# Kernel optimization log

Hardware: AMD Instinct MI355X
Metric: run time of the kernel (lower is better)

The kernel has to match this reference:

```python
import jax, jax.numpy as jnp
import numpy as np

B, T, D_MODEL = 2, 2048, 2048
D_HEAD = 128
H_PER_G = 4
N_GROUPS = D_MODEL // (H_PER_G * D_HEAD)  # 4
ROT_BASE = 10000
EPS = 1e-6


def setup_inputs() -> dict:
    key = jax.random.key(0)
    ks = jax.random.split(key, 5)
    s = D_MODEL ** -0.5
    return {
        "x": jax.random.normal(ks[0], (B, T, D_MODEL), jnp.float32),
        "wq": jax.random.normal(ks[1], (D_MODEL, D_MODEL), jnp.float32) * s,
        "wk": jax.random.normal(ks[2], (D_MODEL, D_MODEL // H_PER_G), jnp.float32) * s,
        "wv": jax.random.normal(ks[3], (D_MODEL, D_MODEL // H_PER_G), jnp.float32) * s,
        "wo": jax.random.normal(ks[4], (D_MODEL, D_MODEL), jnp.float32) * s,
        "gq": jnp.ones((N_GROUPS, H_PER_G, D_HEAD), jnp.float32),
        "gk": jnp.ones((N_GROUPS, D_HEAD), jnp.float32),
    }


def _rmsnorm(t):
    rms = jnp.sqrt(jnp.mean(jnp.square(t), axis=-1, keepdims=True) + EPS)
    return t / rms


def _rope(t):
    # t: [..., length, width]
    length, width = t.shape[-2], t.shape[-1]
    pos = jnp.arange(length)[:, None]                       # [t,1]
    dims = jnp.arange(width // 2)[None, :]                  # [1,d/2]
    ang = jnp.power(float(ROT_BASE), -dims / (width // 2))
    rad = (pos * ang).astype(t.dtype)                       # [t,d/2]
    cos, sin = jnp.cos(rad), jnp.sin(rad)
    even, odd = jnp.split(t, 2, axis=-1)
    return jnp.concatenate([even * cos - odd * sin, even * sin + odd * cos], axis=-1)


def reference(x, wq, wk, wv, wo, gq, gk):
    b, t, _ = x.shape
    q = jnp.einsum('bti,io->bto', x, wq)
    k = jnp.einsum('bti,io->bto', x, wk)
    v = jnp.einsum('bti,io->bto', x, wv)
    # b t (g h d) -> b g h t d ; b t (g d) -> b g t d
    q = q.reshape(b, t, N_GROUPS, H_PER_G, D_HEAD).transpose(0, 2, 3, 1, 4)
    k = k.reshape(b, t, N_GROUPS, D_HEAD).transpose(0, 2, 1, 3)
    v = v.reshape(b, t, N_GROUPS, D_HEAD).transpose(0, 2, 1, 3)
    # QK RMSNorm with gains
    q = _rmsnorm(q) * gq[None, :, :, None, :]
    k = _rmsnorm(k) * gk[None, :, None, :]
    # RoPE
    q = _rope(q)
    k = _rope(k)
    mult = jnp.asarray(D_HEAD ** -0.25, x.dtype)
    s = jnp.einsum('bghid,bgjd->bghij', q * mult, k * mult)
    # causal mask: subtract 1e30 where i < j
    i = jnp.arange(t)[:, None]
    j = jnp.arange(t)[None, :]
    s = s - jnp.asarray(1e30, s.dtype) * (i < j)
    p = jax.nn.softmax(s, axis=-1)
    o = jnp.einsum('bghij,bgjd->bghid', p, v)
    o = o.transpose(0, 3, 1, 2, 4).reshape(b, t, D_MODEL)
    return jnp.einsum('bti,io->bto', o, wo)
```

## Files before the change

### kernel.cpp

```cpp
#include <hip/hip_runtime.h>
#include <cstdint>

typedef unsigned short u16;
typedef __attribute__((ext_vector_type(8))) __bf16 bf16x8;
typedef __attribute__((ext_vector_type(4))) float f32x4;
typedef __attribute__((ext_vector_type(8))) unsigned short u16x8;

#define DEV __device__ __forceinline__

DEV u16 f2bf(float f) {
  __bf16 b = (__bf16)f;
  return __builtin_bit_cast(u16, b);
}
DEV float bf2f(u16 h) { return __uint_as_float(((unsigned)h) << 16); }
DEV float exp2_fast(float x) { float r; asm("v_exp_f32 %0, %1" : "=v"(r) : "v"(x)); return r; }

typedef __attribute__((address_space(1))) void gvoid_t;
typedef __attribute__((address_space(3))) void lvoid_t;

DEV void gload_lds16(const void* g, void* l) {
  __builtin_amdgcn_global_load_lds((gvoid_t*)(void*)(uintptr_t)g,
                                   (lvoid_t*)l, 16, 0, 0);
}

#define B_   2
#define T_   2048
#define DM   2048
#define MROWS (B_*T_)

__global__ void k_convert(const float* __restrict__ in, u16* __restrict__ out, int n4) {
  int i = blockIdx.x * blockDim.x + threadIdx.x;
  if (i >= n4) return;
  float4 v = ((const float4*)in)[i];
  ((ushort4*)out)[i] = make_ushort4(f2bf(v.x), f2bf(v.y), f2bf(v.z), f2bf(v.w));
}

__global__ void k_transpose(const float* __restrict__ in, u16* __restrict__ out, int R, int C) {
  __shared__ float tile[32][33];
  int c0 = blockIdx.x * 32, r0 = blockIdx.y * 32;
  int tx = threadIdx.x, ty = threadIdx.y;
  #pragma unroll
  for (int j = 0; j < 32; j += 8)
    tile[ty + j][tx] = in[(size_t)(r0 + ty + j) * C + c0 + tx];
  __syncthreads();
  #pragma unroll
  for (int j = 0; j < 32; j += 8)
    out[(size_t)(c0 + ty + j) * R + r0 + tx] = f2bf(tile[tx][ty + j]);
}

__global__ void k_rope_table(float2* __restrict__ tab) {
  int i = blockIdx.x * blockDim.x + threadIdx.x;
  int pos = i >> 6, d = i & 63;
  float ang = powf(10000.0f, -(float)d / 64.0f);
  float s, c;
  sincosf((float)pos * ang, &s, &c);
  tab[i] = make_float2(c, s);
}

template <typename OutT>
__global__ __launch_bounds__(256) void k_gemm(
    const u16* __restrict__ A, const u16* __restrict__ BT, OutT* __restrict__ C,
    int M, int N, int K) {
  __shared__ u16 As[128 * 64];
  __shared__ u16 Bs[128 * 64];
  const int tid = threadIdx.x;
  const int w = tid >> 6, lane = tid & 63;
  const int lr = lane & 15, lg = lane >> 4;
  const int m0 = blockIdx.y * 128, n0 = blockIdx.x * 128;
  const int wr = w >> 1, wc = w & 1;
  f32x4 acc[4][4] = {};
  for (int k0 = 0; k0 < K; k0 += 64) {
    __syncthreads();
    #pragma unroll
    for (int i = 0; i < 4; i++) {
      int idx = i * 256 + tid;
      int row = idx >> 3, blk = idx & 7;
      int scol = ((blk ^ (row & 7)) << 3);
      gload_lds16(&A[(size_t)(m0 + row) * K + k0 + scol], &As[(idx & ~63) * 8]);
      gload_lds16(&BT[(size_t)(n0 + row) * K + k0 + scol], &Bs[(idx & ~63) * 8]);
    }
    __syncthreads();
    #pragma unroll
    for (int kk = 0; kk < 2; kk++) {
      bf16x8 af[4], bfr[4];
      #pragma unroll
      for (int m = 0; m < 4; m++) {
        int row = wr * 64 + m * 16 + lr;
        af[m] = *(const bf16x8*)&As[row * 64 + (((kk * 4 + lg) ^ (lr & 7)) << 3)];
      }
      #pragma unroll
      for (int n = 0; n < 4; n++) {
        int row = wc * 64 + n * 16 + lr;
        bfr[n] = *(const bf16x8*)&Bs[row * 64 + (((kk * 4 + lg) ^ (lr & 7)) << 3)];
      }
      #pragma unroll
      for (int m = 0; m < 4; m++)
        #pragma unroll
        for (int n = 0; n < 4; n++)
          acc[m][n] = __builtin_amdgcn_mfma_f32_16x16x32_bf16(af[m], bfr[n], acc[m][n], 0, 0, 0);
    }
  }
  #pragma unroll
  for (int m = 0; m < 4; m++)
    #pragma unroll
    for (int n = 0; n < 4; n++)
      #pragma unroll
      for (int r = 0; r < 4; r++) {
        int row = m0 + wr * 64 + m * 16 + lg * 4 + r;
        int col = n0 + wc * 64 + n * 16 + lr;
        if constexpr (sizeof(OutT) == 2) C[(size_t)row * N + col] = f2bf(acc[m][n][r]);
        else                             C[(size_t)row * N + col] = acc[m][n][r];
      }
}

__global__ void k_norm_rope_q(const u16* __restrict__ qkvf, const float* __restrict__ gq,
                              const float2* __restrict__ tab, u16* __restrict__ qb) {
  int w = threadIdx.x >> 6, lane = threadIdx.x & 63;
  int W = blockIdx.x * 4 + w;
  int h = W & 3, g = (W >> 2) & 3;
  int bt = W >> 4;
  int t = bt & 2047, b = bt >> 11;
  const u16* row = qkvf + (size_t)bt * 3072 + (size_t)(g * 4 + h) * 128;
  float v0 = bf2f(row[lane]);
  float v1 = bf2f(row[lane + 64]);
  float ss = v0 * v0 + v1 * v1;
  #pragma unroll
  for (int off = 1; off < 64; off <<= 1) ss += __shfl_xor(ss, off, 64);
  float inv = 1.0f / sqrtf(ss * (1.0f / 128.0f) + 1e-6f);
  v0 *= inv * gq[(g * 4 + h) * 128 + lane];
  v1 *= inv * gq[(g * 4 + h) * 128 + 64 + lane];
  float2 cs = tab[t * 64 + lane];
  const float sc = 0.1275174f;
  float o0 = (v0 * cs.x - v1 * cs.y) * sc;
  float o1 = (v0 * cs.y + v1 * cs.x) * sc;
  u16* orow = qb + ((size_t)(((b * 4 + g) * 4 + h) * 2048 + t)) * 128;
  orow[lane] = f2bf(o0);
  orow[lane + 64] = f2bf(o1);
}

__global__ void k_norm_rope_k(const u16* __restrict__ qkvf, const float* __restrict__ gk,
                              const float2* __restrict__ tab, u16* __restrict__ kb) {
  int w = threadIdx.x >> 6, lane = threadIdx.x & 63;
  int W = blockIdx.x * 4 + w;
  int g = W & 3;
  int bt = W >> 2;
  int t = bt & 2047, b = bt >> 11;
  const u16* row = qkvf + (size_t)bt * 3072 + 2048 + (size_t)g * 128;
  float v0 = bf2f(row[lane]);
  float v1 = bf2f(row[lane + 64]);
  float ss = v0 * v0 + v1 * v1;
  #pragma unroll
  for (int off = 1; off < 64; off <<= 1) ss += __shfl_xor(ss, off, 64);
  float inv = 1.0f / sqrtf(ss * (1.0f / 128.0f) + 1e-6f);
  v0 *= inv * gk[g * 128 + lane];
  v1 *= inv * gk[g * 128 + 64 + lane];
  float2 cs = tab[t * 64 + lane];
  float o0 = v0 * cs.x - v1 * cs.y;
  float o1 = v0 * cs.y + v1 * cs.x;
  u16* orow = kb + ((size_t)((b * 4 + g) * 2048 + t)) * 128;
  orow[lane] = f2bf(o0);
  orow[lane + 64] = f2bf(o1);
}

__global__ void k_pack_vt(const u16* __restrict__ qkvf, u16* __restrict__ vt) {
  int w = threadIdx.x >> 6, lane = threadIdx.x & 63;
  int W = blockIdx.x * 4 + w;
  int t8 = W & 255, dh = (W >> 8) & 1, bg = W >> 9;
  int b = bg >> 2, g = bg & 3;
  int t0 = t8 * 8;
  int d = dh * 64 + lane;
  u16x8 pack;
  #pragma unroll
  for (int j = 0; j < 8; j++)
    pack[j] = qkvf[(size_t)(b * 2048 + t0 + j) * 3072 + 2560 + g * 128 + d];
  *(u16x8*)&vt[((size_t)(bg * 128 + d)) * 2048 + t0] = pack;
}

DEV void stage_tiles(const u16* kh, const u16* vh, int j0, u16* Kbuf, u16* Vbuf, int tid) {
  #pragma unroll
  for (int i = 0; i < 4; i++) {
    int idx = i * 256 + tid;
    int row = idx >> 4, blk = idx & 15;
    gload_lds16(&kh[(size_t)(j0 + row) * 128 + ((blk ^ (row & 7)) << 3)],
                &Kbuf[(idx & ~63) * 8]);
  }
  #pragma unroll
  for (int i = 0; i < 4; i++) {
    int idx = i * 256 + tid;
    int row = idx >> 3, blk = idx & 7;
    gload_lds16(&vh[(size_t)row * T_ + j0 + ((blk ^ (row & 7)) << 3)],
                &Vbuf[(idx & ~63) * 8]);
  }
}

DEV void attn_tile(const u16* __restrict__ Kc, const u16* __restrict__ Vc,
                   u16* __restrict__ Psw, const bf16x8* qf, f32x4* oacc,
                   float& mrun, float& lsum,
                   int lr, int lg, int w, bool diag) {
  f32x4 s[4] = {};
  #pragma unroll
  for (int kk = 0; kk < 4; kk++) {
    #pragma unroll
    for (int c = 0; c < 4; c++) {
      const int kvr = c * 16 + lr;
      bf16x8 kf = *(const bf16x8*)&Kc[kvr * 128 + (((kk * 4 + lg) ^ (kvr & 7)) << 3)];
      s[c] = __builtin_amdgcn_mfma_f32_16x16x32_bf16(kf, qf[kk], s[c], 0, 0, 0);
    }
  }
  if (diag) {
    #pragma unroll
    for (int c = 0; c < 4; c++)
      #pragma unroll
      for (int r = 0; r < 4; r++)
        if (c * 16 + lg * 4 + r > w * 16 + lr) s[c][r] = -1.0e30f;
  }
  float mx = s[0][0];
  #pragma unroll
  for (int c = 0; c < 4; c++)
    #pragma unroll
    for (int r = 0; r < 4; r++) mx = fmaxf(mx, s[c][r]);
  mx = fmaxf(mx, __shfl_xor(mx, 16, 64));
  mx = fmaxf(mx, __shfl_xor(mx, 32, 64));
  if (!__all(mx <= mrun + 11.0f)) {
    float mnew = fmaxf(mrun, mx);
    float corr = exp2_fast(mrun - mnew);
    mrun = mnew;
    lsum *= corr;
    float cr[4];
    #pragma unroll
    for (int r = 0; r < 4; r++) cr[r] = __shfl(corr, lg * 4 + r, 64);
    #pragma unroll
    for (int nd = 0; nd < 8; nd++) {
      oacc[nd][0] *= cr[0]; oacc[nd][1] *= cr[1];
      oacc[nd][2] *= cr[2]; oacc[nd][3] *= cr[3];
    }
  }
  float rs = 0.f;
  #pragma unroll
  for (int c = 0; c < 4; c++)
    #pragma unroll
    for (int r = 0; r < 4; r++) {
      float pv = exp2_fast(s[c][r] - mrun);
      s[c][r] = pv;
      rs += pv;
    }
  lsum += rs;
  #pragma unroll
  for (int c = 0; c < 4; c++) {
    ushort4 q4 = make_ushort4(f2bf(s[c][0]), f2bf(s[c][1]), f2bf(s[c][2]), f2bf(s[c][3]));
    int blk8 = (c * 4 + lg) ^ ((lr & 7) << 1);
    *(ushort4*)&Psw[lr * 64 + blk8 * 4] = q4;
  }
  #pragma unroll
  for (int ks = 0; ks < 2; ks++) {
    bf16x8 pf = *(const bf16x8*)&Psw[lr * 64 +
                 (((2 * (ks * 4 + lg)) ^ ((lr & 7) << 1)) << 2)];
    #pragma unroll
    for (int nd = 0; nd < 8; nd++) {
      const int d = nd * 16 + lr;
      bf16x8 vf = *(const bf16x8*)&Vc[d * 64 + (((ks * 4 + lg) ^ (d & 7)) << 3)];
      oacc[nd] = __builtin_amdgcn_mfma_f32_16x16x32_bf16(pf, vf, oacc[nd], 0, 0, 0);
    }
  }
}

DEV void attn_epilogue(u16* __restrict__ ob, int b, int g, int h, int q0,
                       const f32x4* oacc, float lsum, int lr, int lg, int w) {
  lsum += __shfl_xor(lsum, 16, 64);
  lsum += __shfl_xor(lsum, 32, 64);
  float inv = 1.0f / lsum;
  float iv[4];
  #pragma unroll
  for (int r = 0; r < 4; r++) iv[r] = __shfl(inv, lg * 4 + r, 64);
  #pragma unroll
  for (int r = 0; r < 4; r++) {
    int orow = q0 + w * 16 + lg * 4 + r;
    size_t base = (size_t)(b * T_ + orow) * 2048 + (size_t)(g * 4 + h) * 128;
    #pragma unroll
    for (int nd = 0; nd < 8; nd++)
      ob[base + nd * 16 + lr] = f2bf(oacc[nd][r] * iv[r]);
  }
}

__global__ __launch_bounds__(256) void k_attn(
    const u16* __restrict__ qb, const u16* __restrict__ kb,
    const u16* __restrict__ vtb, u16* __restrict__ ob) {
  __shared__ __align__(16) u16 Ks[2][64 * 128];
  __shared__ __align__(16) u16 Vs[2][128 * 64];
  __shared__ __align__(16) u16 Ps[4][16 * 64];
  const int head = blockIdx.y;
  const int b = head >> 4, g = (head >> 2) & 3, h = head & 3;
  const int tid = threadIdx.x;
  const int w = tid >> 6, lane = tid & 63;
  const int lr = lane & 15, lg = lane >> 4;
  const u16* qh = qb + (size_t)head * (T_ * 128);
  const u16* kh = kb + (size_t)(b * 4 + g) * (T_ * 128);
  const u16* vh = vtb + (size_t)(b * 4 + g) * (128 * T_);

  #pragma unroll 1
  for (int half = 0; half < 2; ++half) {
    const int qblk = half ? (int)blockIdx.x : 31 - (int)blockIdx.x;
    const int q0 = qblk * 64;
    bf16x8 qf[4];
    const int qrow = q0 + w * 16 + lr;
    #pragma unroll
    for (int kk = 0; kk < 4; kk++)
      qf[kk] = *(const bf16x8*)&qh[(size_t)qrow * 128 + kk * 32 + lg * 8];

    f32x4 oacc[8] = {};
    float mrun = -3.0e38f, lsum = 0.f;

    stage_tiles(kh, vh, 0, Ks[0], Vs[0], tid);
    asm volatile("s_waitcnt vmcnt(0)" ::: "memory");
    __builtin_amdgcn_s_barrier();
    asm volatile("" ::: "memory");
    int cur = 0;
    for (int jt = 0; jt <= qblk; ++jt) {
      if (jt < qblk)
        stage_tiles(kh, vh, (jt + 1) * 64, Ks[cur ^ 1], Vs[cur ^ 1], tid);
      attn_tile(Ks[cur], Vs[cur], Ps[w], qf, oacc, mrun, lsum, lr, lg, w, jt == qblk);
      asm volatile("s_waitcnt vmcnt(0)" ::: "memory");
      __builtin_amdgcn_s_barrier();
      asm volatile("" ::: "memory");
      cur ^= 1;
    }
    attn_epilogue(ob, b, g, h, q0, oacc, lsum, lr, lg, w);
  }
}

#define OFF_XB    ((size_t)0)
#define OFF_WQKVT ((size_t)16777216)
#define OFF_WOT   ((size_t)29360128)
#define OFF_ROPE  ((size_t)37748736)
#define OFF_QB    ((size_t)38797312)
#define OFF_KB    ((size_t)55574528)
#define OFF_VTB   ((size_t)59768832)
#define OFF_QKVF  ((size_t)63963136)
#define OFF_OB    OFF_QKVF

extern "C" void kernel_launch(void* const* d_in, const int* in_sizes, int n_in,
                              void* d_out, int out_size, void* d_ws, size_t ws_size,
                              hipStream_t stream) {
  const float* x  = (const float*)d_in[0];
  const float* wq = (const float*)d_in[1];
  const float* wk = (const float*)d_in[2];
  const float* wv = (const float*)d_in[3];
  const float* wo = (const float*)d_in[4];
  const float* gq = (const float*)d_in[5];
  const float* gk = (const float*)d_in[6];
  float* out = (float*)d_out;
  char* ws = (char*)d_ws;

  u16*    xb    = (u16*)(ws + OFF_XB);
  u16*    wqkvt = (u16*)(ws + OFF_WQKVT);
  u16*    wot   = (u16*)(ws + OFF_WOT);
  float2* rope  = (float2*)(ws + OFF_ROPE);
  u16*    qbuf  = (u16*)(ws + OFF_QB);
  u16*    kbuf  = (u16*)(ws + OFF_KB);
  u16*    vtb   = (u16*)(ws + OFF_VTB);
  u16*    qkvf  = (u16*)(ws + OFF_QKVF);
  u16*    obuf  = (u16*)(ws + OFF_OB);

  k_convert<<<8192, 256, 0, stream>>>(x, xb, (MROWS * DM) / 4);
  k_transpose<<<dim3(64, 64), dim3(32, 8), 0, stream>>>(wq, wqkvt, 2048, 2048);
  k_transpose<<<dim3(16, 64), dim3(32, 8), 0, stream>>>(wk, wqkvt + (size_t)2048 * 2048, 2048, 512);
  k_transpose<<<dim3(16, 64), dim3(32, 8), 0, stream>>>(wv, wqkvt + (size_t)2560 * 2048, 2048, 512);
  k_transpose<<<dim3(64, 64), dim3(32, 8), 0, stream>>>(wo, wot, 2048, 2048);
  k_rope_table<<<512, 256, 0, stream>>>(rope);
  k_gemm<u16><<<dim3(24, 32), 256, 0, stream>>>(xb, wqkvt, qkvf, MROWS, 3072, 2048);
  k_norm_rope_q<<<16384, 256, 0, stream>>>(qkvf, gq, rope, qbuf);
  k_norm_rope_k<<<4096, 256, 0, stream>>>(qkvf, gk, rope, kbuf);
  k_pack_vt<<<1024, 256, 0, stream>>>(qkvf, vtb);
  k_attn<<<dim3(16, 32), 256, 0, stream>>>(qbuf, kbuf, vtb, obuf);
  k_gemm<float><<<dim3(16, 32), 256, 0, stream>>>(obuf, wot, out, MROWS, 2048, 2048);
}
```

Baseline: 226.0 us.

## Use 256x128 GEMM tiles with triple-buffered async loads and setprio around MFMAs

Replaces the 128x128 single-buffered GEMM with a 512-thread, 256x128 tile kernel. It uses three LDS buffers and prefetches two K-tiles ahead, with the loads interleaved between the two MFMA half-steps. It also raises wave priority around MFMA bursts in the GEMM and in the attention tile. The aim is to hide global-load latency and cut per-iteration barrier stalls, at the cost of more LDS (about 144KB), fewer blocks for the projection GEMMs, and fragile hand-written vmcnt accounting.

```diff
diff --git a/kernel.cpp b/kernel.cpp
--- a/kernel.cpp
+++ b/kernel.cpp
@@ -14,6 +14,7 @@
 }
 DEV float bf2f(u16 h) { return __uint_as_float(((unsigned)h) << 16); }
 DEV float exp2_fast(float x) { float r; asm("v_exp_f32 %0, %1" : "=v"(r) : "v"(x)); return r; }
+DEV void barrier_mem() { asm volatile("s_barrier" ::: "memory"); }
 
 typedef __attribute__((address_space(1))) void gvoid_t;
 typedef __attribute__((address_space(3))) void lvoid_t;
@@ -58,56 +59,111 @@
 }
 
 template <typename OutT>
-__global__ __launch_bounds__(256) void k_gemm(
+__global__ __launch_bounds__(512) void k_gemm256(
     const u16* __restrict__ A, const u16* __restrict__ BT, OutT* __restrict__ C,
-    int M, int N, int K) {
-  __shared__ u16 As[128 * 64];
-  __shared__ u16 Bs[128 * 64];
+    int N, int K) {
+  __shared__ __align__(16) u16 As[3][256 * 64];
+  __shared__ __align__(16) u16 Bs[3][128 * 64];
   const int tid = threadIdx.x;
-  const int w = tid >> 6, lane = tid & 63;
+  const int lane = tid & 63;
+  const int w = tid >> 6;
+  const int wrM = w >> 1, wcN = w & 1;
   const int lr = lane & 15, lg = lane >> 4;
-  const int m0 = blockIdx.y * 128, n0 = blockIdx.x * 128;
-  const int wr = w >> 1, wc = w & 1;
+  const int m0 = blockIdx.y * 256, n0 = blockIdx.x * 128;
+  const int NTk = K >> 6;
+
+  auto stageA = [&](int t, int half) {
+    u16* dst = As[t % 3];
+    #pragma unroll
+    for (int i = 0; i < 2; i++) {
+      int idx = half * 1024 + i * 512 + tid;
+      int row = idx >> 3, blk = idx & 7;
+      gload_lds16(&A[(size_t)(m0 + row) * K + t * 64 + ((blk ^ (row & 7)) << 3)],
+                  &dst[(idx & ~63) * 8]);
+    }
+  };
+  auto stageB = [&](int t) {
+    u16* dst = Bs[t % 3];
+    #pragma unroll
+    for (int i = 0; i < 2; i++) {
+      int idx = i * 512 + tid;
+      int row = idx >> 3, blk = idx & 7;
+      gload_lds16(&BT[(size_t)(n0 + row) * K + t * 64 + ((blk ^ (row & 7)) << 3)],
+                  &dst[(idx & ~63) * 8]);
+    }
+  };
+
   f32x4 acc[4][4] = {};
-  for (int k0 = 0; k0 < K; k0 += 64) {
-    __syncthreads();
-    #pragma unroll
-    for (int i = 0; i < 4; i++) {
-      int idx = i * 256 + tid;
-      int row = idx >> 3, blk = idx & 7;
-      int scol = ((blk ^ (row & 7)) << 3);
-      gload_lds16(&A[(size_t)(m0 + row) * K + k0 + scol], &As[(idx & ~63) * 8]);
-      gload_lds16(&BT[(size_t)(n0 + row) * K + k0 + scol], &Bs[(idx & ~63) * 8]);
-    }
-    __syncthreads();
-    #pragma unroll
-    for (int kk = 0; kk < 2; kk++) {
-      bf16x8 af[4], bfr[4];
+
+  stageA(0, 0); stageA(0, 1); stageB(0);
+  stageA(1, 0); stageA(1, 1); stageB(1);
+  asm volatile("s_waitcnt vmcnt(6)" ::: "memory");
+  barrier_mem();
+
+  int bi = 0;
+  for (int t = 0; t < NTk; ++t) {
+    const u16* Ac = As[bi];
+    const u16* Bc = Bs[bi];
+    const bool pf = (t + 2 < NTk);
+    const int tnxt = t + 2;
+    bf16x8 af[4], bg[4];
+    #pragma unroll
+    for (int m = 0; m < 4; m++) {
+      int row = wrM * 64 + m * 16 + lr;
+      af[m] = *(const bf16x8*)&Ac[row * 64 + ((lg ^ (row & 7)) << 3)];
+    }
+    #pragma unroll
+    for (int n = 0; n < 4; n++) {
+      int row = wcN * 64 + n * 16 + lr;
+      bg[n] = *(const bf16x8*)&Bc[row * 64 + ((lg ^ (row & 7)) << 3)];
+    }
+    if (pf) { stageA(tnxt, 0); stageA(tnxt, 1); }
+    barrier_mem();
+    asm volatile("s_waitcnt lgkmcnt(0)" ::: "memory");
+    __builtin_amdgcn_sched_barrier(0);
+    __builtin_amdgcn_s_setprio(1);
+    #pragma unroll
+    for (int m = 0; m < 4; m++)
       #pragma unroll
-      for (int m = 0; m < 4; m++) {
-        int row = wr * 64 + m * 16 + lr;
-        af[m] = *(const bf16x8*)&As[row * 64 + (((kk * 4 + lg) ^ (lr & 7)) << 3)];
-      }
+      for (int n = 0; n < 4; n++)
+        acc[m][n] = __builtin_amdgcn_mfma_f32_16x16x32_bf16(af[m], bg[n], acc[m][n], 0, 0, 0);
+    __builtin_amdgcn_s_setprio(0);
+    barrier_mem();
+    #pragma unroll
+    for (int m = 0; m < 4; m++) {
+      int row = wrM * 64 + m * 16 + lr;
+      af[m] = *(const bf16x8*)&Ac[row * 64 + (((4 + lg) ^ (row & 7)) << 3)];
+    }
+    #pragma unroll
+    for (int n = 0; n < 4; n++) {
+      int row = wcN * 64 + n * 16 + lr;
+      bg[n] = *(const bf16x8*)&Bc[row * 64 + (((4 + lg) ^ (row & 7)) << 3)];
+    }
+    if (pf) stageB(tnxt);
+    barrier_mem();
+    asm volatile("s_waitcnt lgkmcnt(0)" ::: "memory");
+    __builtin_amdgcn_sched_barrier(0);
+    __builtin_amdgcn_s_setprio(1);
+    #pragma unroll
+    for (int m = 0; m < 4; m++)
       #pragma unroll
-      for (int n = 0; n < 4; n++) {
-        int row = wc * 64 + n * 16 + lr;
-        bfr[n] = *(const bf16x8*)&Bs[row * 64 + (((kk * 4 + lg) ^ (lr & 7)) << 3)];
-      }
-      #pragma unroll
-      for (int m = 0; m < 4; m++)
-        #pragma unroll
-        for (int n = 0; n < 4; n++)
-          acc[m][n] = __builtin_amdgcn_mfma_f32_16x16x32_bf16(af[m], bfr[n], acc[m][n], 0, 0, 0);
-    }
-  }
+      for (int n = 0; n < 4; n++)
+        acc[m][n] = __builtin_amdgcn_mfma_f32_16x16x32_bf16(af[m], bg[n], acc[m][n], 0, 0, 0);
+    __builtin_amdgcn_s_setprio(0);
+    if (pf) asm volatile("s_waitcnt vmcnt(6)" ::: "memory");
+    else    asm volatile("s_waitcnt vmcnt(0)" ::: "memory");
+    barrier_mem();
+    bi = (bi == 2) ? 0 : bi + 1;
+  }
+
   #pragma unroll
   for (int m = 0; m < 4; m++)
     #pragma unroll
     for (int n = 0; n < 4; n++)
       #pragma unroll
       for (int r = 0; r < 4; r++) {
-        int row = m0 + wr * 64 + m * 16 + lg * 4 + r;
-        int col = n0 + wc * 64 + n * 16 + lr;
+        int row = m0 + wrM * 64 + m * 16 + lg * 4 + r;
+        int col = n0 + wcN * 64 + n * 16 + lr;
         if constexpr (sizeof(OutT) == 2) C[(size_t)row * N + col] = f2bf(acc[m][n][r]);
         else                             C[(size_t)row * N + col] = acc[m][n][r];
       }
@@ -198,6 +254,7 @@
                    float& mrun, float& lsum,
                    int lr, int lg, int w, bool diag) {
   f32x4 s[4] = {};
+  __builtin_amdgcn_s_setprio(1);
   #pragma unroll
   for (int kk = 0; kk < 4; kk++) {
     #pragma unroll
@@ -207,6 +264,7 @@
       s[c] = __builtin_amdgcn_mfma_f32_16x16x32_bf16(kf, qf[kk], s[c], 0, 0, 0);
     }
   }
+  __builtin_amdgcn_s_setprio(0);
   if (diag) {
     #pragma unroll
     for (int c = 0; c < 4; c++)
@@ -255,12 +313,14 @@
   for (int ks = 0; ks < 2; ks++) {
     bf16x8 pf = *(const bf16x8*)&Psw[lr * 64 +
                  (((2 * (ks * 4 + lg)) ^ ((lr & 7) << 1)) << 2)];
+    __builtin_amdgcn_s_setprio(1);
     #pragma unroll
     for (int nd = 0; nd < 8; nd++) {
       const int d = nd * 16 + lr;
       bf16x8 vf = *(const bf16x8*)&Vc[d * 64 + (((ks * 4 + lg) ^ (d & 7)) << 3)];
       oacc[nd] = __builtin_amdgcn_mfma_f32_16x16x32_bf16(pf, vf, oacc[nd], 0, 0, 0);
     }
+    __builtin_amdgcn_s_setprio(0);
   }
 }
 
@@ -312,16 +372,14 @@
 
     stage_tiles(kh, vh, 0, Ks[0], Vs[0], tid);
     asm volatile("s_waitcnt vmcnt(0)" ::: "memory");
-    __builtin_amdgcn_s_barrier();
-    asm volatile("" ::: "memory");
+    barrier_mem();
     int cur = 0;
     for (int jt = 0; jt <= qblk; ++jt) {
       if (jt < qblk)
         stage_tiles(kh, vh, (jt + 1) * 64, Ks[cur ^ 1], Vs[cur ^ 1], tid);
       attn_tile(Ks[cur], Vs[cur], Ps[w], qf, oacc, mrun, lsum, lr, lg, w, jt == qblk);
       asm volatile("s_waitcnt vmcnt(0)" ::: "memory");
-      __builtin_amdgcn_s_barrier();
-      asm volatile("" ::: "memory");
+      barrier_mem();
       cur ^= 1;
     }
     attn_epilogue(ob, b, g, h, q0, oacc, lsum, lr, lg, w);
@@ -367,10 +425,10 @@
   k_transpose<<<dim3(16, 64), dim3(32, 8), 0, stream>>>(wv, wqkvt + (size_t)2560 * 2048, 2048, 512);
   k_transpose<<<dim3(64, 64), dim3(32, 8), 0, stream>>>(wo, wot, 2048, 2048);
   k_rope_table<<<512, 256, 0, stream>>>(rope);
-  k_gemm<u16><<<dim3(24, 32), 256, 0, stream>>>(xb, wqkvt, qkvf, MROWS, 3072, 2048);
+  k_gemm256<u16><<<dim3(24, 16), 512, 0, stream>>>(xb, wqkvt, qkvf, 3072, 2048);
   k_norm_rope_q<<<16384, 256, 0, stream>>>(qkvf, gq, rope, qbuf);
   k_norm_rope_k<<<4096, 256, 0, stream>>>(qkvf, gk, rope, kbuf);
   k_pack_vt<<<1024, 256, 0, stream>>>(qkvf, vtb);
   k_attn<<<dim3(16, 32), 256, 0, stream>>>(qbuf, kbuf, vtb, obuf);
-  k_gemm<float><<<dim3(16, 32), 256, 0, stream>>>(obuf, wot, out, MROWS, 2048, 2048);
-}
+  k_gemm256<float><<<dim3(16, 16), 512, 0, stream>>>(obuf, wot, out, 2048, 2048);
+}
```

Measured after the change: 231.7 us. 1.03x slower.
